# Optimization experiments

Hardware: AMD Instinct MI355X
Metric: run time of the kernel (lower is better)

Reference implementation:

```python
import jax, jax.numpy as jnp
import numpy as np

N = 100000
E = 1600000
D_IN = 128
HID = 128
N_CLASSES = 40
NEG_SLOPE = 0.2  # PyG GATConv default
BN_EPS = 1e-5


def setup_inputs() -> dict:
    key = jax.random.key(0)
    ks = jax.random.split(key, 16)
    s = 0.1
    return {
        "x": jax.random.normal(ks[0], (N, D_IN), dtype=jnp.float32),
        "edge_index": jax.random.randint(ks[1], (2, E), 0, N, dtype=jnp.int64),
        # GAT layer 1 (in=D_IN, out=HID, heads=1)
        "W1": jax.random.normal(ks[2], (D_IN, HID), dtype=jnp.float32) * s,
        "a_src1": jax.random.normal(ks[3], (HID,), dtype=jnp.float32) * s,
        "a_dst1": jax.random.normal(ks[4], (HID,), dtype=jnp.float32) * s,
        "b1": jnp.zeros((HID,), dtype=jnp.float32),
        # GAT layer 2 (in=HID, out=HID, heads=1)
        "W2": jax.random.normal(ks[5], (HID, HID), dtype=jnp.float32) * s,
        "a_src2": jax.random.normal(ks[6], (HID,), dtype=jnp.float32) * s,
        "a_dst2": jax.random.normal(ks[7], (HID,), dtype=jnp.float32) * s,
        "b2": jnp.zeros((HID,), dtype=jnp.float32),
        # shared BatchNorm1d(HID) applied after every conv
        "gamma": jnp.ones((HID,), dtype=jnp.float32),
        "beta": jnp.zeros((HID,), dtype=jnp.float32),
        # output Linear(HID, N_CLASSES)
        "Wout": jax.random.normal(ks[8], (HID, N_CLASSES), dtype=jnp.float32) * s,
        "bout": jnp.zeros((N_CLASSES,), dtype=jnp.float32),
    }


def reference(x, edge_index, W1, a_src1, a_dst1, b1, W2, a_src2, a_dst2, b2,
              gamma, beta, Wout, bout):
    n = x.shape[0]
    loops = jnp.arange(n, dtype=edge_index.dtype)  # add_self_loops (GATConv default)
    src = jnp.concatenate([edge_index[0], loops])
    dst = jnp.concatenate([edge_index[1], loops])

    def gat_layer(h_in, W, a_s, a_d, b):
        h = h_in @ W                                   # [N, HID]
        e_src = h @ a_s                                # [N] per-node src score
        e_dst = h @ a_d                                # [N] per-node dst score
        e = jax.nn.leaky_relu(e_src[src] + e_dst[dst], NEG_SLOPE)  # [E+N]
        # segment softmax over incoming edges of each dst node
        m = jax.ops.segment_max(e, dst, num_segments=n)
        p = jnp.exp(e - m[dst])
        denom = jax.ops.segment_sum(p, dst, num_segments=n)
        alpha = p / denom[dst]
        out = jax.ops.segment_sum(alpha[:, None] * h[src], dst, num_segments=n)
        return out + b

    def bn_elu(z):
        mu = z.mean(axis=0)
        var = ((z - mu) ** 2).mean(axis=0)  # biased var (BN training mode)
        zh = (z - mu) / jnp.sqrt(var + BN_EPS) * gamma + beta
        return jax.nn.elu(zh)

    h = bn_elu(gat_layer(x, W1, a_src1, a_dst1, b1))
    h = bn_elu(gat_layer(h, W2, a_src2, a_dst2, b2))
    return h @ Wout + bout
```

## Files before the change

### kernel.cpp

```cpp
#include <hip/hip_runtime.h>

#define NNODES 100000
#define NEDGES 1600000
#define ET (NEDGES + NNODES)
#define NBUCK 782
#define NEG 0.2f
#define BNEPS 1e-5f
#define EPB 4096
#define NBLK_E ((ET + EPB - 1) / EPB)

typedef __attribute__((ext_vector_type(8))) short short8;
typedef __attribute__((ext_vector_type(4))) float floatx4;
typedef __attribute__((ext_vector_type(2))) float floatx2;

__device__ __forceinline__ unsigned short f2b(float x) {
    unsigned int u = __float_as_uint(x);
    u += 0x7fff + ((u >> 16) & 1);
    return (unsigned short)(u >> 16);
}
__device__ __forceinline__ float b2f(unsigned short u) {
    return __uint_as_float(((unsigned int)u) << 16);
}
__device__ __forceinline__ float blo2f(unsigned int v) {
    return __uint_as_float(v << 16);
}
__device__ __forceinline__ float bhi2f(unsigned int v) {
    return __uint_as_float(v & 0xffff0000u);
}
__device__ __forceinline__ floatx2 u2f2(unsigned int v) {
    floatx2 r;
    r.x = __uint_as_float(v << 16);
    r.y = __uint_as_float(v & 0xffff0000u);
    return r;
}

__device__ __forceinline__ int edge_src(const int* ei, int e, int w64) {
    if (e >= NEDGES) return e - NEDGES;
    return w64 ? ei[2 * e] : ei[e];
}
__device__ __forceinline__ int edge_dst(const int* ei, int e, int w64) {
    if (e >= NEDGES) return e - NEDGES;
    return w64 ? ei[2 * (NEDGES + e)] : ei[NEDGES + e];
}

__global__ void k_prep(const float* __restrict__ W1, const float* __restrict__ W2,
                       unsigned short* __restrict__ WT1, unsigned short* __restrict__ WT2,
                       const int* ei, int* flag, int* bcnt, int* done, float* bnstat) {
    int t = blockIdx.x * 256 + threadIdx.x;
    if (t < 800) bcnt[t] = 0;
    if (blockIdx.x == 4) {
        bnstat[threadIdx.x] = 0.f;
    } else if (blockIdx.x == 5) {
        bnstat[256 + threadIdx.x] = 0.f;
    }
    if (t == 0) *done = 0;
    if (t == 1) {
        int is64 = 1;
        for (int j = 1; j < 16; j += 2)
            if (ei[j] != 0) is64 = 0;
        *flag = is64;
    }
    int k = t >> 7, n = t & 127;
    WT1[n * 128 + k] = f2b(W1[t]);
    WT2[n * 128 + k] = f2b(W2[t]);
}

__global__ __launch_bounds__(256) void k_bhist(const int* __restrict__ ei,
                                               const int* flag, int* bcnt,
                                               int* done, int* bbase, int* bcur) {
    __shared__ int lc[784];
    __shared__ int sh[256];
    __shared__ int lastf;
    int t = threadIdx.x;
    for (int i = t; i < NBUCK; i += 256) lc[i] = 0;
    __syncthreads();
    int w64 = *flag;
    int base = blockIdx.x * EPB;
    for (int j = 0; j < EPB / 512; j++) {
        int e = base + j * 512 + t * 2;
        if (e + 1 < NEDGES) {
            int d0, d1;
            if (w64) {
                int4 dv = *(const int4*)&ei[2 * (NEDGES + e)];
                d0 = dv.x; d1 = dv.z;
            } else {
                int2 dv = *(const int2*)&ei[NEDGES + e];
                d0 = dv.x; d1 = dv.y;
            }
            atomicAdd(&lc[d0 >> 7], 1);
            atomicAdd(&lc[d1 >> 7], 1);
        } else {
            for (int k = 0; k < 2; k++) {
                int ee = e + k;
                if (ee < ET) atomicAdd(&lc[edge_dst(ei, ee, w64) >> 7], 1);
            }
        }
    }
    __syncthreads();
    for (int i = t; i < NBUCK; i += 256)
        if (lc[i]) atomicAdd(&bcnt[i], lc[i]);
    __threadfence();
    __syncthreads();
    if (t == 0) lastf = (atomicAdd(done, 1) == gridDim.x - 1) ? 1 : 0;
    __syncthreads();
    if (!lastf) return;
    int vals[4], pre[4], sum = 0;
#pragma unroll
    for (int i = 0; i < 4; i++) {
        int id = t * 4 + i;
        int v = (id < NBUCK) ? atomicAdd(&bcnt[id], 0) : 0;
        pre[i] = sum; vals[i] = v; sum += v;
    }
    sh[t] = sum;
    __syncthreads();
    for (int off = 1; off < 256; off <<= 1) {
        int add = (t >= off) ? sh[t - off] : 0;
        __syncthreads();
        sh[t] += add;
        __syncthreads();
    }
    int excl = sh[t] - sum;
#pragma unroll
    for (int i = 0; i < 4; i++) {
        int id = t * 4 + i;
        if (id < NBUCK) { bbase[id] = excl + pre[i]; bcur[id] = excl + pre[i]; }
    }
    if (t == 255) bbase[NBUCK] = sh[255];
    (void)vals;
}

__global__ __launch_bounds__(256) void k_bscatter(const int* __restrict__ ei,
                                                  const int* flag, int* bcur,
                                                  int* __restrict__ pairs) {
    __shared__ int lc[784];
    __shared__ int lbase[784];
    int t = threadIdx.x;
    for (int i = t; i < NBUCK; i += 256) lc[i] = 0;
    __syncthreads();
    int w64 = *flag;
    int base = blockIdx.x * EPB;
    for (int j = 0; j < EPB / 512; j++) {
        int e = base + j * 512 + t * 2;
        if (e + 1 < NEDGES) {
            int d0, d1;
            if (w64) {
                int4 dv = *(const int4*)&ei[2 * (NEDGES + e)];
                d0 = dv.x; d1 = dv.z;
            } else {
                int2 dv = *(const int2*)&ei[NEDGES + e];
                d0 = dv.x; d1 = dv.y;
            }
            atomicAdd(&lc[d0 >> 7], 1);
            atomicAdd(&lc[d1 >> 7], 1);
        } else {
            for (int k = 0; k < 2; k++) {
                int ee = e + k;
                if (ee < ET) atomicAdd(&lc[edge_dst(ei, ee, w64) >> 7], 1);
            }
        }
    }
    __syncthreads();
    for (int i = t; i < NBUCK; i += 256)
        if (lc[i]) lbase[i] = atomicAdd(&bcur[i], lc[i]);
    __syncthreads();
    for (int j = 0; j < EPB / 512; j++) {
        int e = base + j * 512 + t * 2;
        if (e + 1 < NEDGES) {
            int s0, s1, d0, d1;
            if (w64) {
                int4 sv = *(const int4*)&ei[2 * e];
                int4 dv = *(const int4*)&ei[2 * (NEDGES + e)];
                s0 = sv.x; s1 = sv.z; d0 = dv.x; d1 = dv.z;
            } else {
                int2 sv = *(const int2*)&ei[e];
                int2 dv = *(const int2*)&ei[NEDGES + e];
                s0 = sv.x; s1 = sv.y; d0 = dv.x; d1 = dv.y;
            }
            int p0 = atomicAdd(&lbase[d0 >> 7], 1);
            pairs[p0] = (s0 << 7) | (d0 & 127);
            int p1 = atomicAdd(&lbase[d1 >> 7], 1);
            pairs[p1] = (s1 << 7) | (d1 & 127);
        } else {
            for (int k = 0; k < 2; k++) {
                int ee = e + k;
                if (ee < ET) {
                    int src = edge_src(ei, ee, w64);
                    int dst = edge_dst(ei, ee, w64);
                    int pos = atomicAdd(&lbase[dst >> 7], 1);
                    pairs[pos] = (src << 7) | (dst & 127);
                }
            }
        }
    }
}

__global__ __launch_bounds__(256) void k_bsort(const int* __restrict__ pairs,
                                               const int* __restrict__ bbase,
                                               int* __restrict__ rowptr,
                                               int* __restrict__ srcs) {
    __shared__ int ncnt[128];
    __shared__ int nbase[128];
    __shared__ int sscan[128];
    int b = blockIdx.x, t = threadIdx.x;
    if (t < 128) ncnt[t] = 0;
    __syncthreads();
    int s0 = bbase[b], s1 = bbase[b + 1];
    for (int i = s0 + t; i < s1; i += 256)
        atomicAdd(&ncnt[pairs[i] & 127], 1);
    __syncthreads();
    int v = (t < 128) ? ncnt[t] : 0;
    if (t < 128) sscan[t] = v;
    __syncthreads();
    for (int off = 1; off < 128; off <<= 1) {
        int add = (t < 128 && t >= off) ? sscan[t - off] : 0;
        __syncthreads();
        if (t < 128) sscan[t] += add;
        __syncthreads();
    }
    if (t < 128) {
        int excl = sscan[t] - v;
        nbase[t] = excl;
        int node = b * 128 + t;
        if (node <= NNODES) rowptr[node] = s0 + excl;
    }
    __syncthreads();
    if (t < 128) ncnt[t] = nbase[t];
    __syncthreads();
    for (int i = s0 + t; i < s1; i += 256) {
        int pr = pairs[i];
        int off = atomicAdd(&ncnt[pr & 127], 1);
        srcs[s0 + off] = ((unsigned int)pr) >> 7;
    }
}

template<bool BN>
__global__ __launch_bounds__(256) void k_gemm(const void* __restrict__ Ain,
        const unsigned short* __restrict__ WTg,
        const float* __restrict__ sums, const float* __restrict__ sqs,
        const float* __restrict__ gamma, const float* __restrict__ beta,
        const float* __restrict__ a_s, const float* __restrict__ a_d,
        float* __restrict__ es, float* __restrict__ ed,
        unsigned short* __restrict__ hB, int n) {
    __shared__ unsigned short lA[128][136];
    __shared__ unsigned short lW[128][136];
    __shared__ float las[128], lad[128];
    __shared__ float lsc[128], lsh[128];
    int t = threadIdx.x;
    int row0 = blockIdx.x * 128;
    if (t < 128) { las[t] = a_s[t]; lad[t] = a_d[t]; }
    if (BN && t < 128) {
        float mu = sums[t] * (1.f / NNODES);
        float var = fmaxf(sqs[t] * (1.f / NNODES) - mu * mu, 0.f);
        float s = gamma[t] * rsqrtf(var + BNEPS);
        lsc[t] = s;
        lsh[t] = beta[t] - mu * s;
    }

    const uint4* wt4 = (const uint4*)WTg;
#pragma unroll
    for (int j = 0; j < 8; j++) {
        int idx = t + j * 256;
        *(uint4*)&lW[idx >> 4][(idx & 15) * 8] = wt4[idx];
    }
    if (BN) __syncthreads();

    if (BN) {
        const uint4* Ab = (const uint4*)Ain;
#pragma unroll
        for (int j = 0; j < 8; j++) {
            int idx = t + j * 256;
            int r = idx >> 4, seg = idx & 15;
            uint4 v = make_uint4(0, 0, 0, 0);
            if (row0 + r < n) v = Ab[(size_t)(row0 + r) * 16 + seg];
            float f[8];
            f[0] = blo2f(v.x); f[1] = bhi2f(v.x);
            f[2] = blo2f(v.y); f[3] = bhi2f(v.y);
            f[4] = blo2f(v.z); f[5] = bhi2f(v.z);
            f[6] = blo2f(v.w); f[7] = bhi2f(v.w);
            unsigned short us[8];
#pragma unroll
            for (int k = 0; k < 8; k++) {
                int c = seg * 8 + k;
                float z = fmaf(f[k], lsc[c], lsh[c]);
                z = z > 0.f ? z : __expf(z) - 1.f;
                us[k] = f2b(z);
            }
            ushort4 u0, u1;
            u0.x = us[0]; u0.y = us[1]; u0.z = us[2]; u0.w = us[3];
            u1.x = us[4]; u1.y = us[5]; u1.z = us[6]; u1.w = us[7];
            *(ushort4*)&lA[r][seg * 8] = u0;
            *(ushort4*)&lA[r][seg * 8 + 4] = u1;
        }
    } else {
        const float* Af = (const float*)Ain;
#pragma unroll
        for (int j = 0; j < 16; j++) {
            int idx = t + j * 256;
            int r = idx >> 5, c4 = idx & 31;
            float4 v = make_float4(0.f, 0.f, 0.f, 0.f);
            if (row0 + r < n) v = ((const float4*)Af)[(size_t)(row0 + r) * 32 + c4];
            ushort4 u;
            u.x = f2b(v.x); u.y = f2b(v.y); u.z = f2b(v.z); u.w = f2b(v.w);
            *(ushort4*)&lA[r][c4 * 4] = u;
        }
    }
    __syncthreads();

    int w = t >> 6, lane = t & 63;
    int m = lane & 15, q = lane >> 4;
    int ar0 = w * 32 + m, ar1 = w * 32 + 16 + m;
    floatx4 acc0[8], acc1[8];
#pragma unroll
    for (int ct = 0; ct < 8; ct++) { acc0[ct] = (floatx4)0.0f; acc1[ct] = (floatx4)0.0f; }

#pragma unroll
    for (int kt = 0; kt < 4; kt++) {
        int kb = kt * 32 + q * 8;
        short8 af0 = *(const short8*)&lA[ar0][kb];
        short8 af1 = *(const short8*)&lA[ar1][kb];
#pragma unroll
        for (int ct = 0; ct < 8; ct++) {
            short8 bf = *(const short8*)&lW[ct * 16 + m][kb];
            acc0[ct] = __builtin_amdgcn_mfma_f32_16x16x32_bf16(af0, bf, acc0[ct], 0, 0, 0);
            acc1[ct] = __builtin_amdgcn_mfma_f32_16x16x32_bf16(af1, bf, acc1[ct], 0, 0, 0);
        }
    }

    __syncthreads();
#pragma unroll
    for (int ct = 0; ct < 8; ct++)
#pragma unroll
        for (int r = 0; r < 4; r++) {
            lA[w * 32 + q * 4 + r][ct * 16 + m] = f2b(acc0[ct][r]);
            lA[w * 32 + 16 + q * 4 + r][ct * 16 + m] = f2b(acc1[ct][r]);
        }
    __syncthreads();
#pragma unroll
    for (int j = 0; j < 8; j++) {
        int idx = t + j * 256;
        int r = idx >> 4, seg = idx & 15;
        int grow = row0 + r;
        if (grow < n) {
            uint4 v = *(const uint4*)&lA[r][seg * 8];
            ((uint4*)hB)[(size_t)grow * 16 + seg] = v;
        }
    }
    int r = t >> 1, q2 = t & 1;
    float s1 = 0.f, s2 = 0.f;
#pragma unroll
    for (int k = 0; k < 32; k++) {
        int c = q2 * 64 + 2 * k;
        unsigned int u = *(const unsigned int*)&lA[r][c];
        float va = blo2f(u), vb = bhi2f(u);
        s1 += va * las[c] + vb * las[c + 1];
        s2 += va * lad[c] + vb * lad[c + 1];
    }
    s1 += __shfl_xor(s1, 1, 64);
    s2 += __shfl_xor(s2, 1, 64);
    if (q2 == 0 && row0 + r < n) { es[row0 + r] = s1; ed[row0 + r] = s2; }
}

__global__ __launch_bounds__(256) void k_attn(const unsigned short* __restrict__ hB,
                                              const int* __restrict__ srcs,
                                              const int* __restrict__ rowptr,
                                              const float* __restrict__ es,
                                              const float* __restrict__ ed,
                                              const float* __restrict__ bias,
                                              unsigned short* __restrict__ haggB,
                                              int node0, int n) {
    __shared__ uint2 sp[8][32];
    int w = node0 + ((blockIdx.x * 256 + threadIdx.x) >> 5);
    if (w >= n) return;
    int hw = threadIdx.x >> 5;
    int lane32 = threadIdx.x & 31;
    int g = lane32 >> 4, l16 = lane32 & 15;
    int start = rowptr[w], end = rowptr[w + 1];
    float edv = ed[w];
    const uint4* hp4 = (const uint4*)hB;
    floatx2 a0 = {0.f, 0.f}, a1 = {0.f, 0.f}, a2 = {0.f, 0.f}, a3 = {0.f, 0.f};
    float den = 0.f;

    for (int chunk = start; chunk < end; chunk += 32) {
        int i = chunk + lane32;
        int sv = 0; float pv = 0.f;
        if (i < end) {
            sv = srcs[i];
            float e = es[sv] + edv;
            e = e > 0.f ? e : NEG * e;
            pv = __expf(e);
            den += pv;
        }
        sp[hw][lane32] = make_uint2((unsigned)sv, __float_as_uint(pv));
        int cnt = min(32, end - chunk);
        for (int j = 0; j < cnt; j += 8) {
            uint2 e0 = sp[hw][j + g];
            uint2 e1 = sp[hw][j + 2 + g];
            uint2 e2 = sp[hw][j + 4 + g];
            uint2 e3 = sp[hw][j + 6 + g];
            uint4 h0 = hp4[e0.x * 16u + l16];
            uint4 h1 = hp4[e1.x * 16u + l16];
            uint4 h2 = hp4[e2.x * 16u + l16];
            uint4 h3 = hp4[e3.x * 16u + l16];
            float p0 = __uint_as_float(e0.y), p1 = __uint_as_float(e1.y);
            float p2 = __uint_as_float(e2.y), p3 = __uint_as_float(e3.y);
            floatx2 P0 = {p0, p0};
            a0 += P0 * u2f2(h0.x); a1 += P0 * u2f2(h0.y);
            a2 += P0 * u2f2(h0.z); a3 += P0 * u2f2(h0.w);
            floatx2 P1 = {p1, p1};
            a0 += P1 * u2f2(h1.x); a1 += P1 * u2f2(h1.y);
            a2 += P1 * u2f2(h1.z); a3 += P1 * u2f2(h1.w);
            floatx2 P2 = {p2, p2};
            a0 += P2 * u2f2(h2.x); a1 += P2 * u2f2(h2.y);
            a2 += P2 * u2f2(h2.z); a3 += P2 * u2f2(h2.w);
            floatx2 P3 = {p3, p3};
            a0 += P3 * u2f2(h3.x); a1 += P3 * u2f2(h3.y);
            a2 += P3 * u2f2(h3.z); a3 += P3 * u2f2(h3.w);
        }
    }
    den += __shfl_xor(den, 1, 64);  den += __shfl_xor(den, 2, 64);
    den += __shfl_xor(den, 4, 64);  den += __shfl_xor(den, 8, 64);
    den += __shfl_xor(den, 16, 64);
    a0.x += __shfl_xor(a0.x, 16, 64); a0.y += __shfl_xor(a0.y, 16, 64);
    a1.x += __shfl_xor(a1.x, 16, 64); a1.y += __shfl_xor(a1.y, 16, 64);
    a2.x += __shfl_xor(a2.x, 16, 64); a2.y += __shfl_xor(a2.y, 16, 64);
    a3.x += __shfl_xor(a3.x, 16, 64); a3.y += __shfl_xor(a3.y, 16, 64);
    if (g == 0) {
        float inv = 1.f / den;
        const float2* b2p = (const float2*)bias;
        float2 c0 = b2p[l16 * 4 + 0], c1 = b2p[l16 * 4 + 1];
        float2 c2 = b2p[l16 * 4 + 2], c3 = b2p[l16 * 4 + 3];
        uint4 o;
        o.x = (unsigned int)f2b(fmaf(a0.x, inv, c0.x)) |
              ((unsigned int)f2b(fmaf(a0.y, inv, c0.y)) << 16);
        o.y = (unsigned int)f2b(fmaf(a1.x, inv, c1.x)) |
              ((unsigned int)f2b(fmaf(a1.y, inv, c1.y)) << 16);
        o.z = (unsigned int)f2b(fmaf(a2.x, inv, c2.x)) |
              ((unsigned int)f2b(fmaf(a2.y, inv, c2.y)) << 16);
        o.w = (unsigned int)f2b(fmaf(a3.x, inv, c3.x)) |
              ((unsigned int)f2b(fmaf(a3.y, inv, c3.y)) << 16);
        ((uint4*)haggB)[(size_t)w * 16 + l16] = o;
    }
}

__global__ __launch_bounds__(256) void k_bnstats(const unsigned short* __restrict__ hin,
                                                 float* sums, float* sqs, int n) {
    __shared__ float red[4][256];
    int t = threadIdx.x;
    int c2 = t & 63, quarter = t >> 6;
    int r0 = blockIdx.x * 256;
    int rend = min(r0 + 256, n);
    const unsigned int* hp = (const unsigned int*)hin;
    float s0 = 0.f, q0 = 0.f, s1 = 0.f, q1 = 0.f;
    for (int r = r0 + quarter; r < rend; r += 4) {
        unsigned int v = hp[(size_t)r * 64 + c2];
        float a = blo2f(v), b = bhi2f(v);
        s0 += a; q0 += a * a;
        s1 += b; q1 += b * b;
    }
    *(float4*)&red[quarter][c2 * 4] = make_float4(s0, q0, s1, q1);
    __syncthreads();
    float v = red[0][t] + red[1][t] + red[2][t] + red[3][t];
    int c2i = t >> 2, k = t & 3;
    int ch = c2i * 2 + (k >> 1);
    if (k & 1) atomicAdd(&sqs[ch], v);
    else       atomicAdd(&sums[ch], v);
}

__global__ __launch_bounds__(256) void k_outgemm(const unsigned short* __restrict__ h,
                                                 const float* __restrict__ sums,
                                                 const float* __restrict__ sqs,
                                                 const float* __restrict__ gamma,
                                                 const float* __restrict__ beta,
                                                 const float* __restrict__ Wout,
                                                 const float* __restrict__ bout,
                                                 float* __restrict__ out, int n) {
    __shared__ float lwT[40][128];
    __shared__ float lh[64][132];
    __shared__ float lb[40];
    __shared__ float lsc[128], lsh[128];
    int t = threadIdx.x;
    if (t < 128) {
        float mu = sums[t] * (1.f / NNODES);
        float var = fmaxf(sqs[t] * (1.f / NNODES) - mu * mu, 0.f);
        float s = gamma[t] * rsqrtf(var + BNEPS);
        lsc[t] = s;
        lsh[t] = beta[t] - mu * s;
    }
    for (int idx = t; idx < 128 * 40; idx += 256) {
        int r = idx / 40, c = idx % 40;
        lwT[c][r] = Wout[idx];
    }
    if (t < 40) lb[t] = bout[t];
    __syncthreads();
    int n0 = blockIdx.x * 64;
    const uint4* hb4 = (const uint4*)h;
#pragma unroll
    for (int j = 0; j < 4; j++) {
        int idx = t + j * 256;
        int r = idx >> 4, seg = idx & 15;
        uint4 v = make_uint4(0, 0, 0, 0);
        if (n0 + r < n) v = hb4[(size_t)(n0 + r) * 16 + seg];
        float f[8];
        f[0] = blo2f(v.x); f[1] = bhi2f(v.x);
        f[2] = blo2f(v.y); f[3] = bhi2f(v.y);
        f[4] = blo2f(v.z); f[5] = bhi2f(v.z);
        f[6] = blo2f(v.w); f[7] = bhi2f(v.w);
#pragma unroll
        for (int k = 0; k < 8; k++) {
            int c = seg * 8 + k;
            float z = fmaf(f[k], lsc[c], lsh[c]);
            z = z > 0.f ? z : __expf(z) - 1.f;
            lh[r][c] = z;
        }
    }
    __syncthreads();
    int nl = t & 63, g = t >> 6;
    int row = n0 + nl;
    if (row >= n) return;
    float acc[10] = {};
    for (int k = 0; k < 128; k += 4) {
        float4 hv = *(const float4*)&lh[nl][k];
#pragma unroll
        for (int j = 0; j < 10; j++) {
            float4 wv = *(const float4*)&lwT[g * 10 + j][k];
            acc[j] += hv.x * wv.x + hv.y * wv.y + hv.z * wv.z + hv.w * wv.w;
        }
    }
#pragma unroll
    for (int j = 0; j < 10; j++)
        out[(size_t)row * 40 + g * 10 + j] = acc[j] + lb[g * 10 + j];
}

extern "C" void kernel_launch(void* const* d_in, const int* in_sizes, int n_in,
                              void* d_out, int out_size, void* d_ws, size_t ws_size,
                              hipStream_t stream) {
    const float* x      = (const float*)d_in[0];
    const int*   ei     = (const int*)d_in[1];
    const float* W1     = (const float*)d_in[2];
    const float* a_src1 = (const float*)d_in[3];
    const float* a_dst1 = (const float*)d_in[4];
    const float* b1     = (const float*)d_in[5];
    const float* W2     = (const float*)d_in[6];
    const float* a_src2 = (const float*)d_in[7];
    const float* a_dst2 = (const float*)d_in[8];
    const float* b2     = (const float*)d_in[9];
    const float* gamma  = (const float*)d_in[10];
    const float* beta   = (const float*)d_in[11];
    const float* Wout   = (const float*)d_in[12];
    const float* bout   = (const float*)d_in[13];
    float* out = (float*)d_out;

    char* p = (char*)d_ws;
    auto alloc = [&](size_t bytes) -> void* {
        void* r = (void*)p;
        p += (bytes + 255) & ~(size_t)255;
        return r;
    };
    unsigned short* hB    = (unsigned short*)alloc((size_t)NNODES * 128 * 2);
    unsigned short* haggB = (unsigned short*)alloc((size_t)NNODES * 128 * 2);
    float* es     = (float*)alloc((size_t)NNODES * 4);
    float* ed     = (float*)alloc((size_t)NNODES * 4);
    int*   pairs  = (int*)alloc((size_t)ET * 4);
    int*   srcs   = (int*)alloc((size_t)ET * 4);
    int*   rowptr = (int*)alloc((size_t)(NNODES + 1) * 4);
    int*   bcnt   = (int*)alloc(800 * 4);
    int*   bbase  = (int*)alloc(800 * 4);
    int*   bcur   = (int*)alloc(800 * 4);
    float* bnstat = (float*)alloc(4 * 128 * 4);
    unsigned short* WT1 = (unsigned short*)alloc(128 * 128 * 2);
    unsigned short* WT2 = (unsigned short*)alloc(128 * 128 * 2);
    int*   flag   = (int*)alloc(4);
    int*   done   = (int*)alloc(4);

    float* sum1 = bnstat, *sq1 = bnstat + 128, *sum2 = bnstat + 256, *sq2 = bnstat + 384;

    k_prep<<<64, 256, 0, stream>>>(W1, W2, WT1, WT2, ei, flag, bcnt, done, bnstat);
    k_bhist<<<NBLK_E, 256, 0, stream>>>(ei, flag, bcnt, done, bbase, bcur);
    k_bscatter<<<NBLK_E, 256, 0, stream>>>(ei, flag, bcur, pairs);
    k_bsort<<<NBUCK, 256, 0, stream>>>(pairs, bbase, rowptr, srcs);

    const int GB = (NNODES + 127) / 128;
    const int AH = (NNODES / 2) / 8;
    const int SB = (NNODES + 255) / 256;
    const int OB = (NNODES + 63) / 64;

    k_gemm<false><<<GB, 256, 0, stream>>>(x, WT1, nullptr, nullptr, nullptr, nullptr,
                                          a_src1, a_dst1, es, ed, hB, NNODES);
    k_attn<<<AH, 256, 0, stream>>>(hB, srcs, rowptr, es, ed, b1, haggB, 0, NNODES);
    k_attn<<<AH, 256, 0, stream>>>(hB, srcs, rowptr, es, ed, b1, haggB, NNODES / 2, NNODES);
    k_bnstats<<<SB, 256, 0, stream>>>(haggB, sum1, sq1, NNODES);

    k_gemm<true><<<GB, 256, 0, stream>>>(haggB, WT2, sum1, sq1, gamma, beta,
                                         a_src2, a_dst2, es, ed, hB, NNODES);
    k_attn<<<AH, 256, 0, stream>>>(hB, srcs, rowptr, es, ed, b2, haggB, 0, NNODES);
    k_attn<<<AH, 256, 0, stream>>>(hB, srcs, rowptr, es, ed, b2, haggB, NNODES / 2, NNODES);
    k_bnstats<<<SB, 256, 0, stream>>>(haggB, sum2, sq2, NNODES);

    k_outgemm<<<OB, 256, 0, stream>>>(haggB, sum2, sq2, gamma, beta, Wout, bout, out, NNODES);

    (void)in_sizes; (void)n_in; (void)out_size; (void)ws_size;
}
```

Before: 468.5 us.

## Compute output linear layer with one thread per row, reading weights directly from global memory

Rewrites the final BN+ELU+Linear kernel so each thread handles one full node row, keeping all 40 outputs in registers and reading Wout directly from global memory, which is uniform across the wave and cache-resident. This removes the shared-memory staging of the transposed weights and activations, plus one barrier. The aim is to cut LDS traffic and per-block setup. The costs are more registers per thread (40 accumulators), lower occupancy, and uncoalesced per-thread row loads and stores (each thread strides 256 or 160 bytes).

```diff
diff --git a/kernel.cpp b/kernel.cpp
--- a/kernel.cpp
+++ b/kernel.cpp
@@ -474,9 +474,6 @@
                                                  const float* __restrict__ Wout,
                                                  const float* __restrict__ bout,
                                                  float* __restrict__ out, int n) {
-    __shared__ float lwT[40][128];
-    __shared__ float lh[64][132];
-    __shared__ float lb[40];
     __shared__ float lsc[128], lsh[128];
     int t = threadIdx.x;
     if (t < 128) {
@@ -486,20 +483,16 @@
         lsc[t] = s;
         lsh[t] = beta[t] - mu * s;
     }
-    for (int idx = t; idx < 128 * 40; idx += 256) {
-        int r = idx / 40, c = idx % 40;
-        lwT[c][r] = Wout[idx];
-    }
-    if (t < 40) lb[t] = bout[t];
-    __syncthreads();
-    int n0 = blockIdx.x * 64;
+    __syncthreads();
+    int row = blockIdx.x * 256 + t;
+    if (row >= n) return;
     const uint4* hb4 = (const uint4*)h;
-#pragma unroll
-    for (int j = 0; j < 4; j++) {
-        int idx = t + j * 256;
-        int r = idx >> 4, seg = idx & 15;
-        uint4 v = make_uint4(0, 0, 0, 0);
-        if (n0 + r < n) v = hb4[(size_t)(n0 + r) * 16 + seg];
+    float acc[40];
+#pragma unroll
+    for (int j = 0; j < 40; j++) acc[j] = 0.f;
+#pragma unroll
+    for (int seg = 0; seg < 16; seg++) {
+        uint4 v = hb4[(size_t)row * 16 + seg];
         float f[8];
         f[0] = blo2f(v.x); f[1] = bhi2f(v.x);
         f[2] = blo2f(v.y); f[3] = bhi2f(v.y);
@@ -510,25 +503,29 @@
             int c = seg * 8 + k;
             float z = fmaf(f[k], lsc[c], lsh[c]);
             z = z > 0.f ? z : __expf(z) - 1.f;
-            lh[r][c] = z;
-        }
-    }
-    __syncthreads();
-    int nl = t & 63, g = t >> 6;
-    int row = n0 + nl;
-    if (row >= n) return;
-    float acc[10] = {};
-    for (int k = 0; k < 128; k += 4) {
-        float4 hv = *(const float4*)&lh[nl][k];
-#pragma unroll
-        for (int j = 0; j < 10; j++) {
-            float4 wv = *(const float4*)&lwT[g * 10 + j][k];
-            acc[j] += hv.x * wv.x + hv.y * wv.y + hv.z * wv.z + hv.w * wv.w;
-        }
-    }
-#pragma unroll
-    for (int j = 0; j < 10; j++)
-        out[(size_t)row * 40 + g * 10 + j] = acc[j] + lb[g * 10 + j];
+            const float4* wr = (const float4*)(Wout + c * 40);
+#pragma unroll
+            for (int j4 = 0; j4 < 10; j4++) {
+                float4 wv = wr[j4];
+                acc[j4 * 4 + 0] = fmaf(z, wv.x, acc[j4 * 4 + 0]);
+                acc[j4 * 4 + 1] = fmaf(z, wv.y, acc[j4 * 4 + 1]);
+                acc[j4 * 4 + 2] = fmaf(z, wv.z, acc[j4 * 4 + 2]);
+                acc[j4 * 4 + 3] = fmaf(z, wv.w, acc[j4 * 4 + 3]);
+            }
+        }
+    }
+    const float4* b4 = (const float4*)bout;
+    float4* outp = (float4*)(out + (size_t)row * 40);
+#pragma unroll
+    for (int j4 = 0; j4 < 10; j4++) {
+        float4 bv = b4[j4];
+        float4 o;
+        o.x = acc[j4 * 4 + 0] + bv.x;
+        o.y = acc[j4 * 4 + 1] + bv.y;
+        o.z = acc[j4 * 4 + 2] + bv.z;
+        o.w = acc[j4 * 4 + 3] + bv.w;
+        outp[j4] = o;
+    }
 }
 
 extern "C" void kernel_launch(void* const* d_in, const int* in_sizes, int n_in,
@@ -582,7 +579,7 @@
     const int GB = (NNODES + 127) / 128;
     const int AH = (NNODES / 2) / 8;
     const int SB = (NNODES + 255) / 256;
-    const int OB = (NNODES + 63) / 64;
+    const int OB = (NNODES + 255) / 256;
 
     k_gemm<false><<<GB, 256, 0, stream>>>(x, WT1, nullptr, nullptr, nullptr, nullptr,
                                           a_src1, a_dst1, es, ed, hB, NNODES);
```

After: 474.5 us. About the same (+1.3%).
